# Kernel tuning notes

Hardware: AMD Instinct MI355X
Metric: run time of the kernel (lower is better)

Reference implementation:

```python
import jax, jax.numpy as jnp
import numpy as np

N_NODES = 100000
N_EDGES = 3200000
IN_DIM, HD_DIM, OUT_DIM = 128, 64, 32


def setup_inputs() -> dict:
    key = jax.random.key(0)
    ks = jax.random.split(key, 8)
    x = jax.random.normal(ks[0], (N_NODES, IN_DIM), dtype=jnp.float32)
    drop_u = jax.random.uniform(ks[1], (N_NODES, IN_DIM), dtype=jnp.float32)
    adj_val = jax.random.uniform(ks[2], (N_EDGES,), dtype=jnp.float32)
    adj_row = jax.random.randint(ks[3], (N_EDGES,), 0, N_NODES, dtype=jnp.int32)
    adj_col = jax.random.randint(ks[4], (N_EDGES,), 0, N_NODES, dtype=jnp.int32)
    W0 = jax.random.normal(ks[5], (IN_DIM, HD_DIM), dtype=jnp.float32) * (1.0 / np.sqrt(IN_DIM))
    b0 = jnp.zeros((HD_DIM,), dtype=jnp.float32)
    W1 = jax.random.normal(ks[6], (HD_DIM, OUT_DIM), dtype=jnp.float32) * (1.0 / np.sqrt(HD_DIM))
    b1 = jnp.zeros((OUT_DIM,), dtype=jnp.float32)
    return {"x": x, "drop_u": drop_u, "adj_val": adj_val, "adj_row": adj_row,
            "adj_col": adj_col, "W0": W0, "b0": b0, "W1": W1, "b1": b1}


def _spmm(val, row, col, h):
    # sparse [N,N] @ dense [N,D]: out[i] = sum_{e: row[e]=i} val[e] * h[col[e]]
    gathered = val[:, None] * h[col]          # [E, D] irregular gather
    return jax.ops.segment_sum(gathered, row, num_segments=N_NODES)


def reference(x, drop_u, adj_val, adj_row, adj_col, W0, b0, W1, b1):
    # dropout p=0.5 (training): keep where u >= 0.5, scale by 1/(1-p)=2
    mask = (drop_u >= 0.5).astype(x.dtype) * 2.0
    h = x * mask
    h = h @ W0 + b0                     # li0: [N, hd]
    h = _spmm(adj_val, adj_row, adj_col, h)
    h = jax.nn.relu(h)
    h = h @ W1 + b1                     # li1: [N, out]
    out = _spmm(adj_val, adj_row, adj_col, h)
    return out
```

## Files before the change

kernel.cpp:

```cpp
#include <hip/hip_runtime.h>

#define NN 100000
#define NE 3200000
#define EB 4096
#define NBP 782
#define BSH 9
#define BRW 512
#define NBK 196

typedef short short8 __attribute__((ext_vector_type(8)));
typedef float f32x4 __attribute__((ext_vector_type(4)));

static __device__ __forceinline__ unsigned short f2bf(float f) {
  union { float f; unsigned int u; } c; c.f = f;
  unsigned int r = c.u + 0x7FFFu + ((c.u >> 16) & 1u);
  return (unsigned short)(r >> 16);
}
static __device__ __forceinline__ float lo16(unsigned int w) {
  union { unsigned int u; float f; } c; c.u = w << 16; return c.f;
}
static __device__ __forceinline__ float hi16(unsigned int w) {
  union { unsigned int u; float f; } c; c.u = w & 0xFFFF0000u; return c.f;
}


__global__ __launch_bounds__(256) void k_phist(const int* __restrict__ row,
                                               int* __restrict__ bcnt) {
  __shared__ int h[NBK];
  int t = threadIdx.x;
  if (t < NBK) h[t] = 0;
  __syncthreads();
  int e0 = blockIdx.x * EB;
  int n = min(EB, NE - e0);
  for (int i = t; i < n; i += 256) atomicAdd(&h[row[e0 + i] >> BSH], 1);
  __syncthreads();
  if (t < NBK && h[t]) atomicAdd(&bcnt[t], h[t]);
}

__global__ __launch_bounds__(256) void k_bscan(const int* __restrict__ bcnt,
                                               int* __restrict__ bbase,
                                               int* __restrict__ bcur) {
  __shared__ int s[256];
  int t = threadIdx.x;
  int v = (t < NBK) ? bcnt[t] : 0;
  s[t] = v;
  __syncthreads();
  for (int off = 1; off < 256; off <<= 1) {
    int a = (t >= off) ? s[t - off] : 0;
    __syncthreads();
    s[t] += a;
    __syncthreads();
  }
  int ex = s[t] - v;
  if (t < NBK) { bbase[t] = ex; bcur[t] = ex; }
  if (t == NBK - 1) bbase[NBK] = ex + v;
}

__global__ __launch_bounds__(256) void k_part(const int* __restrict__ row,
                                              const int* __restrict__ col,
                                              const float* __restrict__ val,
                                              int* __restrict__ bcur,
                                              uint2* __restrict__ tmp) {
  __shared__ uint2 stage[EB];
  __shared__ int dst[EB];
  __shared__ int h[NBK];
  __shared__ int bex[NBK];
  __shared__ int win[NBK];
  __shared__ int c2[NBK];
  __shared__ int sc[256];
  int t = threadIdx.x;
  int e0 = blockIdx.x * EB;
  int n = min(EB, NE - e0);
  if (t < NBK) { h[t] = 0; c2[t] = 0; }
  __syncthreads();
  for (int i = t; i < n; i += 256) atomicAdd(&h[row[e0 + i] >> BSH], 1);
  __syncthreads();
  int v = (t < NBK) ? h[t] : 0;
  sc[t] = v;
  __syncthreads();
  for (int off = 1; off < 256; off <<= 1) {
    int a = (t >= off) ? sc[t - off] : 0;
    __syncthreads();
    sc[t] += a;
    __syncthreads();
  }
  int ex = sc[t] - v;
  if (t < NBK) {
    bex[t] = ex;
    win[t] = v ? atomicAdd(&bcur[t], v) : 0;
  }
  __syncthreads();
  for (int i = t; i < n; i += 256) {
    int e = e0 + i;
    int r = row[e];
    unsigned int c = (unsigned int)col[e];
    float vv = val[e];
    int b = r >> BSH;
    int rank = atomicAdd(&c2[b], 1);
    int s_ = bex[b] + rank;
    uint2 w;
    w.x = __float_as_uint(vv);
    w.y = ((unsigned int)(r & (BRW - 1)) << 17) | c;
    stage[s_] = w;
    dst[s_] = win[b] + rank;
  }
  __syncthreads();
  for (int i = t; i < n; i += 256) tmp[dst[i]] = stage[i];
}

__global__ __launch_bounds__(512) void k_bsort(const int* __restrict__ bbase,
                                               const uint2* __restrict__ tmp,
                                               uint2* __restrict__ vc,
                                               int* __restrict__ rp) {
  __shared__ int cnt[BRW];
  __shared__ int pre[BRW];
  __shared__ int c2[BRW];
  int t = threadIdx.x;
  int b = blockIdx.x;
  int s0 = bbase[b], s1 = bbase[b + 1];
  int n = s1 - s0;
  cnt[t] = 0; c2[t] = 0;
  __syncthreads();
  for (int i = t; i < n; i += 512) atomicAdd(&cnt[tmp[s0 + i].y >> 17], 1);
  __syncthreads();
  int v = cnt[t];
  pre[t] = v;
  __syncthreads();
  for (int off = 1; off < 512; off <<= 1) {
    int a = (t >= off) ? pre[t - off] : 0;
    __syncthreads();
    pre[t] += a;
    __syncthreads();
  }
  int ex = pre[t] - v;
  int r = (b << BSH) + t;
  if (r < NN) rp[r] = s0 + ex;
  if (b == NBK - 1 && t == 0) rp[NN] = NE;
  pre[t] = ex;
  __syncthreads();
  for (int i = t; i < n; i += 512) {
    uint2 w = tmp[s0 + i];
    int rl = (int)(w.y >> 17);
    int rank = atomicAdd(&c2[rl], 1);
    int pos = s0 + pre[rl] + rank;
    uint2 o;
    o.x = w.x;
    o.y = w.y & 0x1FFFFu;
    vc[pos] = o;
  }
}


__global__ __launch_bounds__(256) void k_wcvt(const float* __restrict__ W0,
                                              unsigned short* __restrict__ W0bT) {
  int t = threadIdx.x;
#pragma unroll
  for (int i = 0; i < 32; ++i) {
    int idx = t + i * 256;
    int n = idx >> 7, k = idx & 127;
    W0bT[idx] = f2bf(W0[(size_t)k * 64 + n]);
  }
}

__global__ __launch_bounds__(256) void k_gemm0(const float* __restrict__ x,
                                               const float* __restrict__ u,
                                               const unsigned short* __restrict__ W0bT,
                                               const float* __restrict__ b0,
                                               unsigned short* __restrict__ h0b) {
  __shared__ unsigned short xs[64][136];
  int t = threadIdx.x;
  int r0 = blockIdx.x * 64;
#pragma unroll
  for (int i = 0; i < 8; ++i) {
    int f4 = t + i * 256;
    int row = f4 >> 5;
    int off = f4 & 31;
    int r = r0 + row;
    float4 m = make_float4(0.f, 0.f, 0.f, 0.f);
    if (r < NN) {
      float4 xv = ((const float4*)(x + (size_t)r * 128))[off];
      float4 uv = ((const float4*)(u + (size_t)r * 128))[off];
      m.x = (uv.x >= 0.5f) ? xv.x : 0.f;
      m.y = (uv.y >= 0.5f) ? xv.y : 0.f;
      m.z = (uv.z >= 0.5f) ? xv.z : 0.f;
      m.w = (uv.w >= 0.5f) ? xv.w : 0.f;
    }
    uint2 pk;
    pk.x = (unsigned int)f2bf(m.x) | ((unsigned int)f2bf(m.y) << 16);
    pk.y = (unsigned int)f2bf(m.z) | ((unsigned int)f2bf(m.w) << 16);
    *(uint2*)&xs[row][off * 4] = pk;
  }
  __syncthreads();

  int lane = t & 63;
  int wv = __builtin_amdgcn_readfirstlane(t >> 6);
  int arow = wv * 16 + (lane & 15);
  int kgrp = lane >> 4;
  int ncol = lane & 15;

  short8 afrag[4];
#pragma unroll
  for (int kb = 0; kb < 4; ++kb)
    afrag[kb] = *(const short8*)&xs[arow][kgrp * 8 + kb * 32];

  short8 bfrag[4][4];
#pragma unroll
  for (int kb = 0; kb < 4; ++kb)
#pragma unroll
    for (int nb = 0; nb < 4; ++nb)
      bfrag[kb][nb] = *(const short8*)&W0bT[(size_t)(nb * 16 + ncol) * 128 +
                                            kgrp * 8 + kb * 32];

  f32x4 acc[4];
#pragma unroll
  for (int nb = 0; nb < 4; ++nb) acc[nb] = (f32x4)(0.f);
#pragma unroll
  for (int kb = 0; kb < 4; ++kb)
#pragma unroll
    for (int nb = 0; nb < 4; ++nb)
      acc[nb] = __builtin_amdgcn_mfma_f32_16x16x32_bf16(afrag[kb], bfrag[kb][nb],
                                                        acc[nb], 0, 0, 0);

#pragma unroll
  for (int nb = 0; nb < 4; ++nb) {
    int c = nb * 16 + ncol;
    float bias = b0[c];
#pragma unroll
    for (int reg = 0; reg < 4; ++reg) {
      int rr = r0 + wv * 16 + kgrp * 4 + reg;
      if (rr < NN) h0b[(size_t)rr * 64 + c] = f2bf(2.f * acc[nb][reg] + bias);
    }
  }
}


__global__ __launch_bounds__(256) void k_gemm1(const unsigned short* __restrict__ s1b,
                                               const float* __restrict__ W1,
                                               const float* __restrict__ b1,
                                               unsigned short* __restrict__ h1b) {
  __shared__ float ss[128][65];
  int t = threadIdx.x;
  int r0 = blockIdx.x * 128;
#pragma unroll
  for (int i = 0; i < 4; ++i) {
    int q = t + i * 256;
    int row = q >> 3;
    int off = q & 7;
    int r = r0 + row;
    float* dp = &ss[row][off * 8];
    if (r < NN) {
      uint4 w = ((const uint4*)(s1b + (size_t)r * 64))[off];
      unsigned int ws[4] = {w.x, w.y, w.z, w.w};
#pragma unroll
      for (int j = 0; j < 4; ++j) {
        dp[2 * j] = lo16(ws[j]);
        dp[2 * j + 1] = hi16(ws[j]);
      }
    } else {
#pragma unroll
      for (int j = 0; j < 8; ++j) dp[j] = 0.f;
    }
  }
  __syncthreads();

  int lane = t & 63;
  int wv = __builtin_amdgcn_readfirstlane(t >> 6);
  int rloc = (wv >> 1) * 64 + lane;
  int dblk = wv & 1;
  int r = r0 + rloc;
  const float* Wd = W1 + dblk * 16;
  float acc[16];
#pragma unroll
  for (int d = 0; d < 16; ++d) acc[d] = 0.f;
#pragma unroll 1
  for (int kc = 0; kc < 4; ++kc) {
    float sm[16];
#pragma unroll
    for (int k = 0; k < 16; ++k) sm[k] = ss[rloc][kc * 16 + k];
#pragma unroll
    for (int k = 0; k < 16; ++k) {
      const float* wrow = Wd + (size_t)(kc * 16 + k) * 32;
#pragma unroll
      for (int d = 0; d < 16; ++d) acc[d] = fmaf(sm[k], wrow[d], acc[d]);
    }
  }
  if (r >= NN) return;
  unsigned int* o32 = (unsigned int*)(h1b + (size_t)r * 32 + dblk * 16);
  const float* bd = b1 + dblk * 16;
#pragma unroll
  for (int d = 0; d < 8; ++d) {
    float a = acc[2 * d] + bd[2 * d];
    float b = acc[2 * d + 1] + bd[2 * d + 1];
    o32[d] = (unsigned int)f2bf(a) | ((unsigned int)f2bf(b) << 16);
  }
}


__global__ __launch_bounds__(256) void k_spmm1(const int* __restrict__ rp,
                                               const uint2* __restrict__ vc,
                                               const uint2* __restrict__ h0v,
                                               uint2* __restrict__ s1v) {
  int wid = (blockIdx.x * 256 + threadIdx.x) >> 6;
  int lane = threadIdx.x & 63;
  if (wid >= NN) return;
  int qw = lane >> 4;
  int d = lane & 15;
  int j0 = rp[wid], j1 = rp[wid + 1];
  float a0 = 0.f, a1 = 0.f, a2 = 0.f, a3 = 0.f;
  int j = j0 + qw;
  uint2 e0, e1, e2, e3;
  bool have = (j + 12 < j1);
  if (have) { e0 = vc[j]; e1 = vc[j + 4]; e2 = vc[j + 8]; e3 = vc[j + 12]; }
  while (have) {
    uint2 g0 = h0v[(size_t)e0.y * 16 + d];
    uint2 g1 = h0v[(size_t)e1.y * 16 + d];
    uint2 g2 = h0v[(size_t)e2.y * 16 + d];
    uint2 g3 = h0v[(size_t)e3.y * 16 + d];
    float v0 = __uint_as_float(e0.x), v1 = __uint_as_float(e1.x);
    float v2 = __uint_as_float(e2.x), v3 = __uint_as_float(e3.x);
    int jn = j + 16;
    bool hn = (jn + 12 < j1);
    if (hn) { e0 = vc[jn]; e1 = vc[jn + 4]; e2 = vc[jn + 8]; e3 = vc[jn + 12]; }
    a0 = fmaf(v0, lo16(g0.x), a0); a1 = fmaf(v0, hi16(g0.x), a1);
    a2 = fmaf(v0, lo16(g0.y), a2); a3 = fmaf(v0, hi16(g0.y), a3);
    a0 = fmaf(v1, lo16(g1.x), a0); a1 = fmaf(v1, hi16(g1.x), a1);
    a2 = fmaf(v1, lo16(g1.y), a2); a3 = fmaf(v1, hi16(g1.y), a3);
    a0 = fmaf(v2, lo16(g2.x), a0); a1 = fmaf(v2, hi16(g2.x), a1);
    a2 = fmaf(v2, lo16(g2.y), a2); a3 = fmaf(v2, hi16(g2.y), a3);
    a0 = fmaf(v3, lo16(g3.x), a0); a1 = fmaf(v3, hi16(g3.x), a1);
    a2 = fmaf(v3, lo16(g3.y), a2); a3 = fmaf(v3, hi16(g3.y), a3);
    j = jn; have = hn;
  }
  for (; j < j1; j += 4) {
    uint2 e = vc[j];
    uint2 g = h0v[(size_t)e.y * 16 + d];
    float v = __uint_as_float(e.x);
    a0 = fmaf(v, lo16(g.x), a0); a1 = fmaf(v, hi16(g.x), a1);
    a2 = fmaf(v, lo16(g.y), a2); a3 = fmaf(v, hi16(g.y), a3);
  }
  a0 += __shfl_xor(a0, 16); a0 += __shfl_xor(a0, 32);
  a1 += __shfl_xor(a1, 16); a1 += __shfl_xor(a1, 32);
  a2 += __shfl_xor(a2, 16); a2 += __shfl_xor(a2, 32);
  a3 += __shfl_xor(a3, 16); a3 += __shfl_xor(a3, 32);
  if (qw == 0) {
    uint2 pk;
    pk.x = (unsigned int)f2bf(fmaxf(a0, 0.f)) | ((unsigned int)f2bf(fmaxf(a1, 0.f)) << 16);
    pk.y = (unsigned int)f2bf(fmaxf(a2, 0.f)) | ((unsigned int)f2bf(fmaxf(a3, 0.f)) << 16);
    s1v[(size_t)wid * 16 + d] = pk;
  }
}

__global__ __launch_bounds__(256) void k_spmm2(const int* __restrict__ rp,
                                               const uint2* __restrict__ vc,
                                               const uint2* __restrict__ h1v,
                                               float* __restrict__ out) {
  int wid = (blockIdx.x * 256 + threadIdx.x) >> 6;
  int lane = threadIdx.x & 63;
  if (wid >= NN) return;
  int slot = lane >> 3;
  int d = lane & 7;
  int j0 = rp[wid], j1 = rp[wid + 1];
  float a0 = 0.f, a1 = 0.f, a2 = 0.f, a3 = 0.f;
  int j = j0 + slot;
  uint2 e0, e1;
  bool have = (j + 8 < j1);
  if (have) { e0 = vc[j]; e1 = vc[j + 8]; }
  while (have) {
    uint2 g0 = h1v[(size_t)e0.y * 8 + d];
    uint2 g1 = h1v[(size_t)e1.y * 8 + d];
    float v0 = __uint_as_float(e0.x), v1 = __uint_as_float(e1.x);
    int jn = j + 16;
    bool hn = (jn + 8 < j1);
    if (hn) { e0 = vc[jn]; e1 = vc[jn + 8]; }
    a0 = fmaf(v0, lo16(g0.x), a0); a1 = fmaf(v0, hi16(g0.x), a1);
    a2 = fmaf(v0, lo16(g0.y), a2); a3 = fmaf(v0, hi16(g0.y), a3);
    a0 = fmaf(v1, lo16(g1.x), a0); a1 = fmaf(v1, hi16(g1.x), a1);
    a2 = fmaf(v1, lo16(g1.y), a2); a3 = fmaf(v1, hi16(g1.y), a3);
    j = jn; have = hn;
  }
  for (; j < j1; j += 8) {
    uint2 e = vc[j];
    uint2 g = h1v[(size_t)e.y * 8 + d];
    float v = __uint_as_float(e.x);
    a0 = fmaf(v, lo16(g.x), a0); a1 = fmaf(v, hi16(g.x), a1);
    a2 = fmaf(v, lo16(g.y), a2); a3 = fmaf(v, hi16(g.y), a3);
  }
  a0 += __shfl_xor(a0, 8); a0 += __shfl_xor(a0, 16); a0 += __shfl_xor(a0, 32);
  a1 += __shfl_xor(a1, 8); a1 += __shfl_xor(a1, 16); a1 += __shfl_xor(a1, 32);
  a2 += __shfl_xor(a2, 8); a2 += __shfl_xor(a2, 16); a2 += __shfl_xor(a2, 32);
  a3 += __shfl_xor(a3, 8); a3 += __shfl_xor(a3, 16); a3 += __shfl_xor(a3, 32);
  if (slot == 0) {
    ((float4*)(out + (size_t)wid * 32))[d] = make_float4(a0, a1, a2, a3);
  }
}


extern "C" void kernel_launch(void* const* d_in, const int* in_sizes, int n_in,
                              void* d_out, int out_size, void* d_ws, size_t ws_size,
                              hipStream_t stream) {
  const float* x   = (const float*)d_in[0];
  const float* u   = (const float*)d_in[1];
  const float* val = (const float*)d_in[2];
  const int* row   = (const int*)d_in[3];
  const int* col   = (const int*)d_in[4];
  const float* W0  = (const float*)d_in[5];
  const float* b0  = (const float*)d_in[6];
  const float* W1  = (const float*)d_in[7];
  const float* b1  = (const float*)d_in[8];
  float* out = (float*)d_out;

  char* p = (char*)d_ws;
  auto take = [&](size_t bytes) {
    char* q = p;
    p += (bytes + 255) & ~(size_t)255;
    return q;
  };
  uint2* tmp = (uint2*)take((size_t)NE * 8);
  uint2* vc  = (uint2*)take((size_t)NE * 8);
  unsigned short* s1b = (unsigned short*)take((size_t)NN * 64 * 2);
  int* rp    = (int*)take((size_t)(NN + 1) * 4);
  int* bcnt  = (int*)take((size_t)NBK * 4);
  int* bbase = (int*)take((size_t)(NBK + 1) * 4);
  int* bcur  = (int*)take((size_t)NBK * 4);
  unsigned short* w0bt = (unsigned short*)take((size_t)64 * 128 * 2);
  unsigned short* h0b = (unsigned short*)tmp;
  unsigned short* h1b = (unsigned short*)((char*)tmp + (size_t)NN * 64 * 2);

  hipMemsetAsync(bcnt, 0, (size_t)NBK * 4, stream);
  k_phist<<<NBP, 256, 0, stream>>>(row, bcnt);
  k_bscan<<<1, 256, 0, stream>>>(bcnt, bbase, bcur);
  k_part<<<NBP, 256, 0, stream>>>(row, col, val, bcur, tmp);
  k_bsort<<<NBK, 512, 0, stream>>>(bbase, tmp, vc, rp);

  k_wcvt<<<1, 256, 0, stream>>>(W0, w0bt);
  k_gemm0<<<(NN + 63) / 64, 256, 0, stream>>>(x, u, w0bt, b0, h0b);
  k_spmm1<<<(NN + 3) / 4, 256, 0, stream>>>(rp, vc, (const uint2*)h0b,
                                            (uint2*)s1b);
  k_gemm1<<<(NN + 127) / 128, 256, 0, stream>>>(s1b, W1, b1, h1b);
  k_spmm2<<<(NN + 3) / 4, 256, 0, stream>>>(rp, vc, (const uint2*)h1b, out);
}
```

Before: 260.5 us.

## Fuse second dense layer into first SpMM epilogue via wave shuffles

Removes the separate k_gemm1 kernel and the bf16 intermediate s1b. After each wave reduces its 64-wide row of the first SpMM and applies ReLU, it computes the 64x32 product with W1 through lane shuffles and writes h1b directly. This drops one kernel launch and a full write-then-read of the N x 64 intermediate. In exchange every wave does 32 shuffle+FMA steps with W1 reads from cache, which adds work to the gather-bound SpMM. It also skips the bf16 rounding of the ReLU output, which slightly changes numerics.

```diff
diff --git a/kernel.cpp b/kernel.cpp
--- a/kernel.cpp
+++ b/kernel.cpp
@@ -233,73 +233,12 @@
   }
 }
 
-
-__global__ __launch_bounds__(256) void k_gemm1(const unsigned short* __restrict__ s1b,
+__global__ __launch_bounds__(256) void k_spmm1(const int* __restrict__ rp,
+                                               const uint2* __restrict__ vc,
+                                               const uint2* __restrict__ h0v,
                                                const float* __restrict__ W1,
                                                const float* __restrict__ b1,
                                                unsigned short* __restrict__ h1b) {
-  __shared__ float ss[128][65];
-  int t = threadIdx.x;
-  int r0 = blockIdx.x * 128;
-#pragma unroll
-  for (int i = 0; i < 4; ++i) {
-    int q = t + i * 256;
-    int row = q >> 3;
-    int off = q & 7;
-    int r = r0 + row;
-    float* dp = &ss[row][off * 8];
-    if (r < NN) {
-      uint4 w = ((const uint4*)(s1b + (size_t)r * 64))[off];
-      unsigned int ws[4] = {w.x, w.y, w.z, w.w};
-#pragma unroll
-      for (int j = 0; j < 4; ++j) {
-        dp[2 * j] = lo16(ws[j]);
-        dp[2 * j + 1] = hi16(ws[j]);
-      }
-    } else {
-#pragma unroll
-      for (int j = 0; j < 8; ++j) dp[j] = 0.f;
-    }
-  }
-  __syncthreads();
-
-  int lane = t & 63;
-  int wv = __builtin_amdgcn_readfirstlane(t >> 6);
-  int rloc = (wv >> 1) * 64 + lane;
-  int dblk = wv & 1;
-  int r = r0 + rloc;
-  const float* Wd = W1 + dblk * 16;
-  float acc[16];
-#pragma unroll
-  for (int d = 0; d < 16; ++d) acc[d] = 0.f;
-#pragma unroll 1
-  for (int kc = 0; kc < 4; ++kc) {
-    float sm[16];
-#pragma unroll
-    for (int k = 0; k < 16; ++k) sm[k] = ss[rloc][kc * 16 + k];
-#pragma unroll
-    for (int k = 0; k < 16; ++k) {
-      const float* wrow = Wd + (size_t)(kc * 16 + k) * 32;
-#pragma unroll
-      for (int d = 0; d < 16; ++d) acc[d] = fmaf(sm[k], wrow[d], acc[d]);
-    }
-  }
-  if (r >= NN) return;
-  unsigned int* o32 = (unsigned int*)(h1b + (size_t)r * 32 + dblk * 16);
-  const float* bd = b1 + dblk * 16;
-#pragma unroll
-  for (int d = 0; d < 8; ++d) {
-    float a = acc[2 * d] + bd[2 * d];
-    float b = acc[2 * d + 1] + bd[2 * d + 1];
-    o32[d] = (unsigned int)f2bf(a) | ((unsigned int)f2bf(b) << 16);
-  }
-}
-
-
-__global__ __launch_bounds__(256) void k_spmm1(const int* __restrict__ rp,
-                                               const uint2* __restrict__ vc,
-                                               const uint2* __restrict__ h0v,
-                                               uint2* __restrict__ s1v) {
   int wid = (blockIdx.x * 256 + threadIdx.x) >> 6;
   int lane = threadIdx.x & 63;
   if (wid >= NN) return;
@@ -342,13 +281,23 @@
   a1 += __shfl_xor(a1, 16); a1 += __shfl_xor(a1, 32);
   a2 += __shfl_xor(a2, 16); a2 += __shfl_xor(a2, 32);
   a3 += __shfl_xor(a3, 16); a3 += __shfl_xor(a3, 32);
-  if (qw == 0) {
-    uint2 pk;
-    pk.x = (unsigned int)f2bf(fmaxf(a0, 0.f)) | ((unsigned int)f2bf(fmaxf(a1, 0.f)) << 16);
-    pk.y = (unsigned int)f2bf(fmaxf(a2, 0.f)) | ((unsigned int)f2bf(fmaxf(a3, 0.f)) << 16);
-    s1v[(size_t)wid * 16 + d] = pk;
-  }
-}
+  float r_[4];
+  r_[0] = fmaxf(a0, 0.f); r_[1] = fmaxf(a1, 0.f);
+  r_[2] = fmaxf(a2, 0.f); r_[3] = fmaxf(a3, 0.f);
+
+  int c = lane & 31;
+  int half8 = (lane >> 5) * 8;
+  const float* W1p = W1 + (lane >> 5) * 1024 + c;
+  float hacc = 0.f;
+#pragma unroll
+  for (int k = 0; k < 32; ++k) {
+    float sv = __shfl(r_[k & 3], (k >> 2) + half8);
+    hacc = fmaf(sv, W1p[k * 32], hacc);
+  }
+  hacc += __shfl_xor(hacc, 32);
+  if (lane < 32) h1b[(size_t)wid * 32 + c] = f2bf(hacc + b1[c]);
+}
+
 
 __global__ __launch_bounds__(256) void k_spmm2(const int* __restrict__ rp,
                                                const uint2* __restrict__ vc,
@@ -417,7 +366,6 @@
   };
   uint2* tmp = (uint2*)take((size_t)NE * 8);
   uint2* vc  = (uint2*)take((size_t)NE * 8);
-  unsigned short* s1b = (unsigned short*)take((size_t)NN * 64 * 2);
   int* rp    = (int*)take((size_t)(NN + 1) * 4);
   int* bcnt  = (int*)take((size_t)NBK * 4);
   int* bbase = (int*)take((size_t)(NBK + 1) * 4);
@@ -434,8 +382,6 @@
 
   k_wcvt<<<1, 256, 0, stream>>>(W0, w0bt);
   k_gemm0<<<(NN + 63) / 64, 256, 0, stream>>>(x, u, w0bt, b0, h0b);
-  k_spmm1<<<(NN + 3) / 4, 256, 0, stream>>>(rp, vc, (const uint2*)h0b,
-                                            (uint2*)s1b);
-  k_gemm1<<<(NN + 127) / 128, 256, 0, stream>>>(s1b, W1, b1, h1b);
+  k_spmm1<<<(NN + 3) / 4, 256, 0, stream>>>(rp, vc, (const uint2*)h0b, W1, b1, h1b);
   k_spmm2<<<(NN + 3) / 4, 256, 0, stream>>>(rp, vc, (const uint2*)h1b, out);
 }
```

After: 265.9 us. +2.1%, slower.
